# Kernel optimization log

Hardware: AMD Instinct MI355X
Metric: run time of the kernel (lower is better)

Reference implementation:

```python
import jax, jax.numpy as jnp
import numpy as np
from jax import lax

B, T, HID = 2, 2048, 2048
H, DK, DV = 16, 64, 128          # num_heads, head_k_dim, head_v_dim
C = 16                            # chunk_size (hardcoded in module __call__)
LOWR = 16                         # gate_low_rank_dim
NORMALIZER = 16.0                 # gate_logit_normalizer
EPS = 1e-5
SCALE = DK ** -0.5


def setup_inputs() -> dict:
    key = jax.random.key(0)
    ks = jax.random.split(key, 9)
    def w(k, shape):
        return jax.random.normal(k, shape, jnp.float32) * (shape[0] ** -0.5)
    return {
        "hidden_states": jax.random.normal(ks[0], (B, T, HID), jnp.float32),
        "Wq": w(ks[1], (HID, H * DK)),
        "Wk": w(ks[2], (HID, H * DK)),
        "Wv": w(ks[3], (HID, H * DV)),
        "Wg": w(ks[4], (HID, H * DV)),
        "Wgk1": w(ks[5], (HID, LOWR)),
        "Wgk2": w(ks[6], (LOWR, H * DK)),
        "bgk2": jnp.zeros((H * DK,), jnp.float32),
        "Wo": w(ks[7], (H * DV, HID)),
        "norm_w": jnp.ones((DV,), jnp.float32),
    }


def _chunk_gla(q, k, v, gk):
    """Chunked gated linear attention.
    q,k,gk: [B,T,H,DK], v: [B,T,H,DV]; gk is log-decay (<= 0).
    Recurrence: S_t = diag(exp(gk_t)) S_{t-1} + k_t^T v_t ; o_t = scale * q_t S_t.
    """
    b, t, h, dk = q.shape
    dv = v.shape[-1]
    n = t // C
    def to_chunks(x):  # [B,T,H,d] -> [B,H,N,C,d]
        return x.reshape(b, n, C, h, x.shape[-1]).transpose(0, 3, 1, 2, 4)
    q, k, v, gk = map(to_chunks, (q, k, v, gk))

    gc = jnp.cumsum(gk, axis=3)                 # within-chunk cumulative log-decay
    qe = q * jnp.exp(gc) * SCALE                # decay-weighted queries
    ke = k * jnp.exp(-gc)                       # inverse-decay keys (safe for C=16)
    # intra-chunk causal attention: A[i,j] = sum_d q_i k_j exp(gc_i - gc_j), j<=i
    A = jnp.einsum('bhncd,bhnmd->bhncm', qe, ke)
    A = jnp.where(jnp.tril(jnp.ones((C, C), bool)), A, 0.0)
    o_intra = jnp.einsum('bhncm,bhnme->bhnce', A, v)

    g_last = gc[:, :, :, -1:, :]                # [B,H,N,1,DK]
    k_dec = k * jnp.exp(g_last - gc)            # keys decayed to end of chunk
    kv = jnp.einsum('bhncd,bhnce->bhnde', k_dec, v)   # per-chunk state increment
    decay = jnp.exp(g_last[:, :, :, 0, :])      # [B,H,N,DK] total chunk decay

    def step(S, inp):  # S: [B,H,DK,DV]
        qe_c, kv_c, dec_c = inp
        o_c = jnp.einsum('bhcd,bhde->bhce', qe_c, S)
        return dec_c[..., None] * S + kv_c, o_c

    S0 = jnp.zeros((b, h, dk, dv), q.dtype)
    xs = (qe.transpose(2, 0, 1, 3, 4), kv.transpose(2, 0, 1, 3, 4), decay.transpose(2, 0, 1, 3))
    _, o_inter = lax.scan(step, S0, xs)          # [N,B,H,C,DV]

    o = o_intra + o_inter.transpose(1, 2, 0, 3, 4)
    return o.transpose(0, 2, 3, 1, 4).reshape(b, t, h, dv)  # [B,T,H,DV]


def reference(hidden_states, Wq, Wk, Wv, Wg, Wgk1, Wgk2, bgk2, Wo, norm_w):
    x = hidden_states
    q = (x @ Wq).reshape(B, T, H, DK)
    k = (x @ Wk).reshape(B, T, H, DK)
    v = (x @ Wv).reshape(B, T, H, DV)
    gk = jax.nn.log_sigmoid((x @ Wgk1) @ Wgk2 + bgk2) / NORMALIZER
    gk = gk.reshape(B, T, H, DK)

    o = _chunk_gla(q, k, v, gk)                  # [B,T,H,DV]

    # FusedRMSNormGated: rmsnorm(o) * weight, gated by swish(g) per head
    g = (x @ Wg).reshape(B, T, H, DV)
    o = o * lax.rsqrt(jnp.mean(o * o, axis=-1, keepdims=True) + EPS) * norm_w
    o = o * (g * jax.nn.sigmoid(g))
    return o.reshape(B, T, H * DV) @ Wo
```

## Files before the change

kernel.cpp:

```cpp
#include <hip/hip_runtime.h>
#include <hip/hip_bf16.h>
#include <math.h>

#define B_    2
#define T_    2048
#define HID_  2048
#define H_    16
#define DK_   64
#define DV_   128
#define CC    16
#define NCHUNK (T_/CC)
#define NSEG  16
#define M_    (B_*T_)
#define SCALE_ 0.125f

typedef __attribute__((ext_vector_type(8))) __bf16 bf16x8;
typedef __attribute__((ext_vector_type(8))) unsigned short u16x8;
typedef __attribute__((ext_vector_type(4))) float f32x4;

__device__ __forceinline__ unsigned short f2bf(float f) {
  unsigned int u = __float_as_uint(f);
  u += 0x7fff + ((u >> 16) & 1);
  return (unsigned short)(u >> 16);
}
__device__ __forceinline__ float bf2f(unsigned short u) {
  return __uint_as_float(((unsigned int)u) << 16);
}

typedef const __attribute__((address_space(1))) void* as1cv;
typedef __attribute__((address_space(3))) void* as3v;
__device__ __forceinline__ void gload16(const void* g, void* l) {
  __builtin_amdgcn_global_load_lds((as1cv)g, (as3v)l, 16, 0, 0);
}

__global__ __launch_bounds__(256) void prep_kernel(const float* __restrict__ x,
                                                   unsigned short* __restrict__ xb,
                                                   const float* __restrict__ Wq,
                                                   const float* __restrict__ Wk,
                                                   const float* __restrict__ Wv,
                                                   const float* __restrict__ Wg,
                                                   const float* __restrict__ Wo,
                                                   unsigned short* __restrict__ WqkT,
                                                   unsigned short* __restrict__ WvgT,
                                                   unsigned short* __restrict__ WoT) {
  const int t = threadIdx.x;
  int id = blockIdx.x;
  if (id < 2048) {
    const float4* x4 = reinterpret_cast<const float4*>(x);
    ushort4* o4 = reinterpret_cast<ushort4*>(xb);
    const int base = id * 1024 + t;
    float4 f0 = x4[base];
    float4 f1 = x4[base + 256];
    float4 f2 = x4[base + 512];
    float4 f3 = x4[base + 768];
    ushort4 u0 = {f2bf(f0.x), f2bf(f0.y), f2bf(f0.z), f2bf(f0.w)};
    ushort4 u1 = {f2bf(f1.x), f2bf(f1.y), f2bf(f1.z), f2bf(f1.w)};
    ushort4 u2 = {f2bf(f2.x), f2bf(f2.y), f2bf(f2.z), f2bf(f2.w)};
    ushort4 u3 = {f2bf(f3.x), f2bf(f3.y), f2bf(f3.z), f2bf(f3.w)};
    o4[base] = u0; o4[base + 256] = u1; o4[base + 512] = u2; o4[base + 768] = u3;
    return;
  }
  id -= 2048;
  const float* in; unsigned short* out; int N;
  if (id < 512)        { in = Wq; out = WqkT;                         N = 1024; }
  else if (id < 1024)  { in = Wk; out = WqkT + (size_t)1024*2048;     N = 1024; id -= 512; }
  else if (id < 2048)  { in = Wv; out = WvgT;                         N = 2048; id -= 1024; }
  else if (id < 3072)  { in = Wg; out = WvgT + (size_t)2048*2048;     N = 2048; id -= 2048; }
  else                 { in = Wo; out = WoT;                          N = 2048; id -= 3072; }
  const int nx = N / 64;
  const int n0 = (id % nx) * 64;
  const int k0 = (id / nx) * 64;
  __shared__ float tl[64][65];
  const int kr = t >> 4;
  const int nq = t & 15;
  #pragma unroll
  for (int it = 0; it < 4; ++it) {
    int kk = it*16 + kr;
    float4 v = *reinterpret_cast<const float4*>(&in[(size_t)(k0 + kk) * N + n0 + nq*4]);
    tl[kk][nq*4+0] = v.x; tl[kk][nq*4+1] = v.y;
    tl[kk][nq*4+2] = v.z; tl[kk][nq*4+3] = v.w;
  }
  __syncthreads();
  const int nr = t >> 3;
  const int kq = t & 7;
  #pragma unroll
  for (int it = 0; it < 2; ++it) {
    int nn = it*32 + nr;
    u16x8 u;
    #pragma unroll
    for (int r = 0; r < 8; ++r) u[r] = f2bf(tl[kq*8 + r][nn]);
    *reinterpret_cast<u16x8*>(&out[(size_t)(n0 + nn) * 2048 + k0 + kq*8]) = u;
  }
}

__global__ __launch_bounds__(256) void lr_kernel(const float* __restrict__ x,
                                                 const float* __restrict__ w1,
                                                 const float* __restrict__ w2,
                                                 const float* __restrict__ bias,
                                                 float* __restrict__ gkout) {
  const int row0 = blockIdx.x * 4;
  const int t = threadIdx.x;
  __shared__ float part[4][4][17];
  __shared__ float t1s[4][16];
  const int r    = t >> 6;
  const int lane = t & 63;
  const int j    = lane & 15;
  const int p    = lane >> 4;
  const float* xr = x + (size_t)(row0 + r) * HID_;
  float acc = 0.f;
  const int k0 = p * 512;
  for (int kk = k0; kk < k0 + 512; kk += 4) {
    float4 xv = *reinterpret_cast<const float4*>(&xr[kk]);
    acc = fmaf(xv.x, w1[(kk+0)*16 + j], acc);
    acc = fmaf(xv.y, w1[(kk+1)*16 + j], acc);
    acc = fmaf(xv.z, w1[(kk+2)*16 + j], acc);
    acc = fmaf(xv.w, w1[(kk+3)*16 + j], acc);
  }
  part[r][p][j] = acc;
  __syncthreads();
  if (t < 64) {
    int rr = t >> 4, jj = t & 15;
    t1s[rr][jj] = part[rr][0][jj] + part[rr][1][jj] + part[rr][2][jj] + part[rr][3][jj];
  }
  __syncthreads();
  #pragma unroll
  for (int i = 0; i < 4; ++i) {
    int n = t + i * 256;
    float b0 = bias[n];
    float a0 = b0, a1 = b0, a2 = b0, a3 = b0;
    #pragma unroll
    for (int jj = 0; jj < 16; ++jj) {
      float wv = w2[jj * 1024 + n];
      a0 = fmaf(t1s[0][jj], wv, a0);
      a1 = fmaf(t1s[1][jj], wv, a1);
      a2 = fmaf(t1s[2][jj], wv, a2);
      a3 = fmaf(t1s[3][jj], wv, a3);
    }
    gkout[(size_t)(row0+0)*1024 + n] = (fminf(a0,0.f) - log1pf(expf(-fabsf(a0)))) * (1.f/16.f);
    gkout[(size_t)(row0+1)*1024 + n] = (fminf(a1,0.f) - log1pf(expf(-fabsf(a1)))) * (1.f/16.f);
    gkout[(size_t)(row0+2)*1024 + n] = (fminf(a2,0.f) - log1pf(expf(-fabsf(a2)))) * (1.f/16.f);
    gkout[(size_t)(row0+3)*1024 + n] = (fminf(a3,0.f) - log1pf(expf(-fabsf(a3)))) * (1.f/16.f);
  }
}

template<bool OBF>
__global__ __launch_bounds__(512, 2) void gemm256(const unsigned short* __restrict__ A,
                                                  const unsigned short* __restrict__ Bt,
                                                  void* __restrict__ Cv,
                                                  int M, int N, int K) {
  __shared__ char ldsb[131072];
  const int t    = threadIdx.x;
  const int lane = t & 63;
  const int wid  = t >> 6;
  const int wr   = wid >> 2;
  const int wc   = wid & 3;
  const int lr   = lane & 15;
  const int lk   = lane >> 4;
  int flat = blockIdx.y * gridDim.x + blockIdx.x;
  if (gridDim.x * gridDim.y == 256) flat = (flat & 7) * 32 + (flat >> 3);
  const int row0 = (flat / gridDim.x) * 256;
  const int col0 = (flat % gridDim.x) * 256;
  const int NKT  = K >> 6;
  const size_t K2 = (size_t)K * 2;

  const int r_s  = t >> 2;
  const int kx_s = ((t & 3) * 16) ^ (((t >> 5) & 1) << 5);

  const int ha = wr;
  const int hb = wc >> 1;
  const int rbl = (wc & 1) * 64;

  f32x4 acc[8][4];
  #pragma unroll
  for (int m = 0; m < 8; ++m)
    #pragma unroll
    for (int n = 0; n < 4; ++n) acc[m][n] = (f32x4){0.f, 0.f, 0.f, 0.f};

  auto stage_half = [&](int p, int o, int h, int kt) {
    const char* src = o ? (const char*)Bt : (const char*)A;
    const int R0 = (o ? col0 : row0) + h * 128;
    const char* g = src + (size_t)(R0 + r_s) * K2 + (size_t)kt * 128 + kx_s;
    char* l = ldsb + ((((p << 1) | o) << 1 | h) << 14) + t * 16;
    gload16(g, l);
    gload16(g + 64, l + 8192);
  };
  auto lda = [&](int p, int mf, int ks) -> bf16x8 {
    int r = mf * 16 + lr;
    int a = ((((p << 1) | 0) << 1 | ha) << 14) + ks * 8192 + r * 64 + lk * 16;
    a ^= ((r >> 3) & 1) << 5;
    return *(const bf16x8*)(ldsb + a);
  };
  auto ldb = [&](int p, int nf, int ks) -> bf16x8 {
    int r = rbl + nf * 16 + lr;
    int a = ((((p << 1) | 1) << 1 | hb) << 14) + ks * 8192 + r * 64 + lk * 16;
    a ^= ((r >> 3) & 1) << 5;
    return *(const bf16x8*)(ldsb + a);
  };

  stage_half(0, 1, 0, 0); stage_half(0, 1, 1, 0);
  stage_half(0, 0, 0, 0); stage_half(0, 0, 1, 0);
  if (1 < NKT) {
    stage_half(1, 1, 0, 1); stage_half(1, 1, 1, 1);
    stage_half(1, 0, 0, 1); stage_half(1, 0, 1, 1);
  }
  __builtin_amdgcn_sched_barrier(0);
  asm volatile("s_waitcnt vmcnt(8)" ::: "memory");
  __builtin_amdgcn_sched_barrier(0);
  __builtin_amdgcn_s_barrier();

  bf16x8 fa[4][2], fb[2][2], fb2[2][2];

  for (int kt = 0; kt < NKT; ++kt) {
    const int p = kt & 1;
    const bool st = (kt + 2 < NKT);
    #pragma unroll
    for (int m = 0; m < 4; ++m) { fa[m][0] = lda(p, m, 0); fa[m][1] = lda(p, m, 1); }
    __builtin_amdgcn_sched_barrier(0);
    #pragma unroll
    for (int n = 0; n < 2; ++n) { fb[n][0] = ldb(p, n, 0); fb[n][1] = ldb(p, n, 1); }
    __builtin_amdgcn_sched_barrier(0);
    #pragma unroll
    for (int n = 0; n < 2; ++n) { fb2[n][0] = ldb(p, n + 2, 0); fb2[n][1] = ldb(p, n + 2, 1); }
    __builtin_amdgcn_sched_barrier(0);
    asm volatile("s_waitcnt lgkmcnt(4)" ::: "memory");
    __builtin_amdgcn_sched_barrier(0);
    __builtin_amdgcn_s_setprio(1);
    #pragma unroll
    for (int m = 0; m < 4; ++m)
      #pragma unroll
      for (int n = 0; n < 2; ++n) {
        acc[m][n] = __builtin_amdgcn_mfma_f32_16x16x32_bf16(fa[m][0], fb[n][0], acc[m][n], 0, 0, 0);
        acc[m][n] = __builtin_amdgcn_mfma_f32_16x16x32_bf16(fa[m][1], fb[n][1], acc[m][n], 0, 0, 0);
      }
    __builtin_amdgcn_s_setprio(0);
    __builtin_amdgcn_sched_barrier(0);
    asm volatile("s_waitcnt lgkmcnt(0)" ::: "memory");
    __builtin_amdgcn_sched_barrier(0);
    __builtin_amdgcn_s_setprio(1);
    #pragma unroll
    for (int m = 0; m < 4; ++m)
      #pragma unroll
      for (int n = 0; n < 2; ++n) {
        acc[m][n+2] = __builtin_amdgcn_mfma_f32_16x16x32_bf16(fa[m][0], fb2[n][0], acc[m][n+2], 0, 0, 0);
        acc[m][n+2] = __builtin_amdgcn_mfma_f32_16x16x32_bf16(fa[m][1], fb2[n][1], acc[m][n+2], 0, 0, 0);
      }
    __builtin_amdgcn_s_setprio(0);
    __builtin_amdgcn_sched_barrier(0);
    __builtin_amdgcn_s_barrier();
    if (st) { stage_half(p, 1, 0, kt + 2); stage_half(p, 1, 1, kt + 2); }
    __builtin_amdgcn_sched_barrier(0);
    #pragma unroll
    for (int m = 0; m < 4; ++m) { fa[m][0] = lda(p, m + 4, 0); fa[m][1] = lda(p, m + 4, 1); }
    __builtin_amdgcn_sched_barrier(0);
    asm volatile("s_waitcnt lgkmcnt(0)" ::: "memory");
    __builtin_amdgcn_sched_barrier(0);
    __builtin_amdgcn_s_setprio(1);
    #pragma unroll
    for (int m = 0; m < 4; ++m)
      #pragma unroll
      for (int n = 0; n < 2; ++n) {
        acc[m+4][n] = __builtin_amdgcn_mfma_f32_16x16x32_bf16(fa[m][0], fb[n][0], acc[m+4][n], 0, 0, 0);
        acc[m+4][n] = __builtin_amdgcn_mfma_f32_16x16x32_bf16(fa[m][1], fb[n][1], acc[m+4][n], 0, 0, 0);
      }
    #pragma unroll
    for (int m = 0; m < 4; ++m)
      #pragma unroll
      for (int n = 0; n < 2; ++n) {
        acc[m+4][n+2] = __builtin_amdgcn_mfma_f32_16x16x32_bf16(fa[m][0], fb2[n][0], acc[m+4][n+2], 0, 0, 0);
        acc[m+4][n+2] = __builtin_amdgcn_mfma_f32_16x16x32_bf16(fa[m][1], fb2[n][1], acc[m+4][n+2], 0, 0, 0);
      }
    __builtin_amdgcn_s_setprio(0);
    __builtin_amdgcn_sched_barrier(0);
    __builtin_amdgcn_s_barrier();
    if (st) { stage_half(p, 0, 0, kt + 2); stage_half(p, 0, 1, kt + 2); }
    __builtin_amdgcn_sched_barrier(0);
    if (kt == NKT - 2) asm volatile("s_waitcnt vmcnt(0)" ::: "memory");
    else               asm volatile("s_waitcnt vmcnt(8)" ::: "memory");
    __builtin_amdgcn_sched_barrier(0);
    __builtin_amdgcn_s_barrier();
  }

  #pragma unroll
  for (int m = 0; m < 8; ++m) {
    int row = row0 + wr*128 + m*16 + lk*4;
    #pragma unroll
    for (int n = 0; n < 4; ++n) {
      int col = col0 + wc*64 + n*16 + lr;
      #pragma unroll
      for (int j = 0; j < 4; ++j) {
        if (OBF) ((unsigned short*)Cv)[(size_t)(row + j) * N + col] = f2bf(acc[m][n][j]);
        else     ((float*)Cv)[(size_t)(row + j) * N + col] = acc[m][n][j];
      }
    }
  }
}

template<bool OBF>
__global__ __launch_bounds__(512, 2) void gemm256x128(const unsigned short* __restrict__ A,
                                                      const unsigned short* __restrict__ Bt,
                                                      void* __restrict__ Cv,
                                                      int M, int N, int K) {
  __shared__ char ldsb[98304];
  const int t    = threadIdx.x;
  const int lane = t & 63;
  const int wid  = t >> 6;
  const int wr   = wid >> 1;
  const int wc   = wid & 1;
  const int lr   = lane & 15;
  const int lk   = lane >> 4;
  int flat = blockIdx.y * gridDim.x + blockIdx.x;
  if (gridDim.x * gridDim.y == 256) flat = (flat & 7) * 32 + (flat >> 3);
  const int row0 = (flat / gridDim.x) * 256;
  const int col0 = (flat % gridDim.x) * 128;
  const int NKT  = K >> 6;
  const size_t K2 = (size_t)K * 2;

  const int r_s  = t >> 2;
  const int kx_s = ((t & 3) * 16) ^ (((t >> 5) & 1) << 5);

  const int ha  = wr >> 1;
  const int ral = (wr & 1) * 64;
  const int rbl = wc * 64;

  f32x4 acc[4][4];
  #pragma unroll
  for (int m = 0; m < 4; ++m)
    #pragma unroll
    for (int n = 0; n < 4; ++n) acc[m][n] = (f32x4){0.f, 0.f, 0.f, 0.f};

  auto stage_slot = [&](int p, int slot, int kt) {
    const char* src = (slot == 2) ? (const char*)Bt : (const char*)A;
    const int R0 = (slot == 2) ? col0 : (row0 + slot * 128);
    const char* g = src + (size_t)(R0 + r_s) * K2 + (size_t)kt * 128 + kx_s;
    char* l = ldsb + p * 49152 + slot * 16384 + t * 16;
    gload16(g, l);
    gload16(g + 64, l + 8192);
  };
  auto lda = [&](int p, int mf, int ks) -> bf16x8 {
    int r = ral + mf * 16 + lr;
    int a = p * 49152 + ha * 16384 + ks * 8192 + r * 64 + lk * 16;
    a ^= ((r >> 3) & 1) << 5;
    return *(const bf16x8*)(ldsb + a);
  };
  auto ldb = [&](int p, int nf, int ks) -> bf16x8 {
    int r = rbl + nf * 16 + lr;
    int a = p * 49152 + 32768 + ks * 8192 + r * 64 + lk * 16;
    a ^= ((r >> 3) & 1) << 5;
    return *(const bf16x8*)(ldsb + a);
  };

  stage_slot(0, 2, 0); stage_slot(0, 0, 0); stage_slot(0, 1, 0);
  if (1 < NKT) { stage_slot(1, 2, 1); stage_slot(1, 0, 1); stage_slot(1, 1, 1); }
  __builtin_amdgcn_sched_barrier(0);
  asm volatile("s_waitcnt vmcnt(6)" ::: "memory");
  __builtin_amdgcn_sched_barrier(0);
  __builtin_amdgcn_s_barrier();

  bf16x8 fa[2][2], fb[2][2], fb2[2][2];

  for (int kt = 0; kt < NKT; ++kt) {
    const int p = kt & 1;
    const bool st = (kt + 2 < NKT);
    #pragma unroll
    for (int m = 0; m < 2; ++m) { fa[m][0] = lda(p, m, 0); fa[m][1] = lda(p, m, 1); }
    __builtin_amdgcn_sched_barrier(0);
    #pragma unroll
    for (int n = 0; n < 2; ++n) { fb[n][0] = ldb(p, n, 0); fb[n][1] = ldb(p, n, 1); }
    __builtin_amdgcn_sched_barrier(0);
    #pragma unroll
    for (int n = 0; n < 2; ++n) { fb2[n][0] = ldb(p, n + 2, 0); fb2[n][1] = ldb(p, n + 2, 1); }
    __builtin_amdgcn_sched_barrier(0);
    asm volatile("s_waitcnt lgkmcnt(4)" ::: "memory");
    __builtin_amdgcn_sched_barrier(0);
    __builtin_amdgcn_s_setprio(1);
    #pragma unroll
    for (int m = 0; m < 2; ++m)
      #pragma unroll
      for (int n = 0; n < 2; ++n) {
        acc[m][n] = __builtin_amdgcn_mfma_f32_16x16x32_bf16(fa[m][0], fb[n][0], acc[m][n], 0, 0, 0);
        acc[m][n] = __builtin_amdgcn_mfma_f32_16x16x32_bf16(fa[m][1], fb[n][1], acc[m][n], 0, 0, 0);
      }
    __builtin_amdgcn_s_setprio(0);
    __builtin_amdgcn_sched_barrier(0);
    asm volatile("s_waitcnt lgkmcnt(0)" ::: "memory");
    __builtin_amdgcn_sched_barrier(0);
    __builtin_amdgcn_s_setprio(1);
    #pragma unroll
    for (int m = 0; m < 2; ++m)
      #pragma unroll
      for (int n = 0; n < 2; ++n) {
        acc[m][n+2] = __builtin_amdgcn_mfma_f32_16x16x32_bf16(fa[m][0], fb2[n][0], acc[m][n+2], 0, 0, 0);
        acc[m][n+2] = __builtin_amdgcn_mfma_f32_16x16x32_bf16(fa[m][1], fb2[n][1], acc[m][n+2], 0, 0, 0);
      }
    __builtin_amdgcn_s_setprio(0);
    __builtin_amdgcn_sched_barrier(0);
    __builtin_amdgcn_s_barrier();
    if (st) stage_slot(p, 2, kt + 2);
    __builtin_amdgcn_sched_barrier(0);
    #pragma unroll
    for (int m = 0; m < 2; ++m) { fa[m][0] = lda(p, m + 2, 0); fa[m][1] = lda(p, m + 2, 1); }
    __builtin_amdgcn_sched_barrier(0);
    asm volatile("s_waitcnt lgkmcnt(0)" ::: "memory");
    __builtin_amdgcn_sched_barrier(0);
    __builtin_amdgcn_s_setprio(1);
    #pragma unroll
    for (int m = 0; m < 2; ++m)
      #pragma unroll
      for (int n = 0; n < 2; ++n) {
        acc[m+2][n] = __builtin_amdgcn_mfma_f32_16x16x32_bf16(fa[m][0], fb[n][0], acc[m+2][n], 0, 0, 0);
        acc[m+2][n] = __builtin_amdgcn_mfma_f32_16x16x32_bf16(fa[m][1], fb[n][1], acc[m+2][n], 0, 0, 0);
      }
    #pragma unroll
    for (int m = 0; m < 2; ++m)
      #pragma unroll
      for (int n = 0; n < 2; ++n) {
        acc[m+2][n+2] = __builtin_amdgcn_mfma_f32_16x16x32_bf16(fa[m][0], fb2[n][0], acc[m+2][n+2], 0, 0, 0);
        acc[m+2][n+2] = __builtin_amdgcn_mfma_f32_16x16x32_bf16(fa[m][1], fb2[n][1], acc[m+2][n+2], 0, 0, 0);
      }
    __builtin_amdgcn_s_setprio(0);
    __builtin_amdgcn_sched_barrier(0);
    __builtin_amdgcn_s_barrier();
    if (st) { stage_slot(p, 0, kt + 2); stage_slot(p, 1, kt + 2); }
    __builtin_amdgcn_sched_barrier(0);
    if (kt == NKT - 2) asm volatile("s_waitcnt vmcnt(0)" ::: "memory");
    else               asm volatile("s_waitcnt vmcnt(6)" ::: "memory");
    __builtin_amdgcn_sched_barrier(0);
    __builtin_amdgcn_s_barrier();
  }

  #pragma unroll
  for (int m = 0; m < 4; ++m) {
    int row = row0 + wr*64 + m*16 + lk*4;
    #pragma unroll
    for (int n = 0; n < 4; ++n) {
      int col = col0 + wc*64 + n*16 + lr;
      #pragma unroll
      for (int j = 0; j < 4; ++j) {
        if (OBF) ((unsigned short*)Cv)[(size_t)(row + j) * N + col] = f2bf(acc[m][n][j]);
        else     ((float*)Cv)[(size_t)(row + j) * N + col] = acc[m][n][j];
      }
    }
  }
}

__global__ __launch_bounds__(256) void gla_phase_a(const float* __restrict__ qk,
                                                   const unsigned short* __restrict__ vg,
                                                   const float* __restrict__ gk,
                                                   float* __restrict__ Sseg,
                                                   float* __restrict__ Dseg) {
  const int seg = blockIdx.x & 15;
  const int h   = (blockIdx.x >> 4) & 15;
  const int b   = blockIdx.x >> 8;
  const int t    = threadIdx.x;
  const int lane = t & 63;
  const int wid  = t >> 6;
  const int q    = lane >> 4;
  const int lr   = lane & 15;
  __shared__ float gc[16][68];
  __shared__ float dec_[64];
  __shared__ unsigned short kdT[64][40];
  __shared__ unsigned short vvT[128][40];

  for (int i = t; i < 1024; i += 256) kdT[i >> 4][16 + (i & 15)] = 0;
  for (int i = t; i < 2048; i += 256) vvT[i >> 4][16 + (i & 15)] = 0;

  f32x4 s_reg[2][4];
  #pragma unroll
  for (int et = 0; et < 2; ++et)
    #pragma unroll
    for (int dt = 0; dt < 4; ++dt) s_reg[et][dt] = (f32x4){0.f,0.f,0.f,0.f};
  float gt = 0.f;

  for (int c8 = 0; c8 < NCHUNK/NSEG; ++c8) {
    const int ch = seg * (NCHUNK/NSEG) + c8;
    __syncthreads();
    {
      float acc = 0.f;
      #pragma unroll
      for (int c = 0; c < CC; ++c) {
        acc += gk[((size_t)(b*T_ + ch*CC + c)) * 1024 + h*DK_ + lane];
        gc[c][lane] = acc;
      }
      gt += acc;
      dec_[lane] = expf(acc);
    }
    __syncthreads();
    {
      int c = t >> 4, d0 = (t & 15) * 4;
      float4 k4 = *reinterpret_cast<const float4*>(
          &qk[((size_t)(b*T_ + ch*CC + c)) * 2048 + 1024 + h*DK_ + d0]);
      float ka[4] = {k4.x, k4.y, k4.z, k4.w};
      #pragma unroll
      for (int j = 0; j < 4; ++j)
        kdT[d0 + j][c] = f2bf(ka[j] * expf(gc[CC-1][d0 + j] - gc[c][d0 + j]));
    }
    {
      int c = t & 15, e0 = (t >> 4) * 8;
      const ushort4* vp = reinterpret_cast<const ushort4*>(
          &vg[((size_t)(b*T_ + ch*CC + c)) * 4096 + h*DV_ + e0]);
      ushort4 a = vp[0], bb = vp[1];
      vvT[e0+0][c] = a.x;  vvT[e0+1][c] = a.y;  vvT[e0+2][c] = a.z;  vvT[e0+3][c] = a.w;
      vvT[e0+4][c] = bb.x; vvT[e0+5][c] = bb.y; vvT[e0+6][c] = bb.z; vvT[e0+7][c] = bb.w;
    }
    __syncthreads();
    bf16x8 vf[2], kf[4];
    #pragma unroll
    for (int et = 0; et < 2; ++et)
      vf[et] = *(const bf16x8*)&vvT[wid*32 + et*16 + lr][q*8];
    #pragma unroll
    for (int dt = 0; dt < 4; ++dt)
      kf[dt] = *(const bf16x8*)&kdT[dt*16 + lr][q*8];
    #pragma unroll
    for (int et = 0; et < 2; ++et)
      #pragma unroll
      for (int dt = 0; dt < 4; ++dt) {
        f32x4 dl = __builtin_amdgcn_mfma_f32_16x16x32_bf16(vf[et], kf[dt],
                     (f32x4){0.f,0.f,0.f,0.f}, 0, 0, 0);
        float dv = dec_[dt*16 + lr];
        #pragma unroll
        for (int j = 0; j < 4; ++j)
          s_reg[et][dt][j] = fmaf(s_reg[et][dt][j], dv, dl[j]);
      }
  }
  const size_t base = ((size_t)((b*H_ + h)*NSEG + seg)) * (DK_*DV_);
  #pragma unroll
  for (int et = 0; et < 2; ++et)
    #pragma unroll
    for (int dt = 0; dt < 4; ++dt)
      #pragma unroll
      for (int j = 0; j < 4; ++j)
        Sseg[base + (size_t)(wid*32 + et*16 + q*4 + j) * 64 + dt*16 + lr] = s_reg[et][dt][j];
  if (t < 64)
    Dseg[(size_t)((b*H_ + h)*NSEG + seg) * DK_ + t] = expf(gt);
}

__global__ __launch_bounds__(256) void gla_combine(float* __restrict__ Sseg,
                                                   const float* __restrict__ Dseg) {
  const int bh = blockIdx.x;
  const int t = threadIdx.x;
  __shared__ float Dl[64];
  float4 S_run[8];
  #pragma unroll
  for (int j = 0; j < 8; ++j) S_run[j] = (float4){0.f,0.f,0.f,0.f};
  const int d0 = (t * 4) & 63;
  for (int seg = 0; seg < NSEG; ++seg) {
    const size_t base = ((size_t)bh*NSEG + seg) * (DK_*DV_);
    if (t < 64) Dl[t] = Dseg[((size_t)bh*NSEG + seg) * DK_ + t];
    __syncthreads();
    #pragma unroll
    for (int j = 0; j < 8; ++j) {
      int idx = j*1024 + t*4;
      float4 sl = *reinterpret_cast<float4*>(&Sseg[base + idx]);
      *reinterpret_cast<float4*>(&Sseg[base + idx]) = S_run[j];
      S_run[j].x = fmaf(Dl[d0+0], S_run[j].x, sl.x);
      S_run[j].y = fmaf(Dl[d0+1], S_run[j].y, sl.y);
      S_run[j].z = fmaf(Dl[d0+2], S_run[j].z, sl.z);
      S_run[j].w = fmaf(Dl[d0+3], S_run[j].w, sl.w);
    }
    __syncthreads();
  }
}

__global__ __launch_bounds__(256) void gla_phase_c(const float* __restrict__ qk,
                                                   const unsigned short* __restrict__ vg,
                                                   const float* __restrict__ gk,
                                                   const float* __restrict__ Sseg,
                                                   const float* __restrict__ norm_w,
                                                   unsigned short* __restrict__ yb) {
  const int seg = blockIdx.x & 15;
  const int h   = (blockIdx.x >> 4) & 15;
  const int b   = blockIdx.x >> 8;
  const int t    = threadIdx.x;
  const int lane = t & 63;
  const int wid  = t >> 6;
  const int q    = lane >> 4;
  const int lr   = lane & 15;
  __shared__ float gc[16][68];
  __shared__ float dec_[64];
  __shared__ unsigned short qe[16][72];
  __shared__ unsigned short ke[16][72];
  __shared__ unsigned short kdT[64][40];
  __shared__ unsigned short vvT[128][40];
  __shared__ unsigned short Am[16][40];
  __shared__ unsigned short Sb[128][72];
  __shared__ float ss_lds[4][16];
  __shared__ float nw[128];

  for (int i = t; i < 1024; i += 256) kdT[i >> 4][16 + (i & 15)] = 0;
  for (int i = t; i < 2048; i += 256) vvT[i >> 4][16 + (i & 15)] = 0;
  if (t < 256) { int c = t >> 4, m = t & 15; Am[c][16 + m] = 0; }
  if (t < 128) nw[t] = norm_w[t];

  f32x4 s_reg[2][4];
  const size_t sbase = ((size_t)((b*H_ + h)*NSEG + seg)) * (DK_*DV_);
  #pragma unroll
  for (int et = 0; et < 2; ++et)
    #pragma unroll
    for (int dt = 0; dt < 4; ++dt)
      #pragma unroll
      for (int j = 0; j < 4; ++j) {
        int e = wid*32 + et*16 + q*4 + j, d = dt*16 + lr;
        float v = Sseg[sbase + (size_t)e * 64 + d];
        s_reg[et][dt][j] = v;
        Sb[e][d] = f2bf(v);
      }

  for (int c8 = 0; c8 < NCHUNK/NSEG; ++c8) {
    const int ch = seg * (NCHUNK/NSEG) + c8;
    __syncthreads();
    {
      float acc = 0.f;
      #pragma unroll
      for (int c = 0; c < CC; ++c) {
        acc += gk[((size_t)(b*T_ + ch*CC + c)) * 1024 + h*DK_ + lane];
        gc[c][lane] = acc;
      }
      dec_[lane] = expf(acc);
    }
    __syncthreads();
    {
      int c = t >> 4, d0 = (t & 15) * 4;
      const size_t gbq = ((size_t)(b*T_ + ch*CC + c)) * 2048 + h*DK_ + d0;
      float4 q4 = *reinterpret_cast<const float4*>(&qk[gbq]);
      float4 k4 = *reinterpret_cast<const float4*>(&qk[gbq + 1024]);
      float qa[4] = {q4.x, q4.y, q4.z, q4.w};
      float ka[4] = {k4.x, k4.y, k4.z, k4.w};
      ushort4 qw, kw;
      unsigned short* qwp = (unsigned short*)&qw;
      unsigned short* kwp = (unsigned short*)&kw;
      #pragma unroll
      for (int j = 0; j < 4; ++j) {
        float gcv = gc[c][d0 + j];
        float gl  = gc[CC-1][d0 + j];
        qwp[j] = f2bf(qa[j] * expf(gcv) * SCALE_);
        kwp[j] = f2bf(ka[j] * expf(-gcv));
        kdT[d0 + j][c] = f2bf(ka[j] * expf(gl - gcv));
      }
      *reinterpret_cast<ushort4*>(&qe[c][d0]) = qw;
      *reinterpret_cast<ushort4*>(&ke[c][d0]) = kw;
    }
    {
      int c = t & 15, e0 = (t >> 4) * 8;
      const ushort4* vp = reinterpret_cast<const ushort4*>(
          &vg[((size_t)(b*T_ + ch*CC + c)) * 4096 + h*DV_ + e0]);
      ushort4 a = vp[0], bb = vp[1];
      vvT[e0+0][c] = a.x;  vvT[e0+1][c] = a.y;  vvT[e0+2][c] = a.z;  vvT[e0+3][c] = a.w;
      vvT[e0+4][c] = bb.x; vvT[e0+5][c] = bb.y; vvT[e0+6][c] = bb.z; vvT[e0+7][c] = bb.w;
    }
    __syncthreads();
    bf16x8 qA0 = *(const bf16x8*)&qe[lr][q*8];
    bf16x8 qA1 = *(const bf16x8*)&qe[lr][32 + q*8];
    {
      bf16x8 kB0 = *(const bf16x8*)&ke[lr][q*8];
      bf16x8 kB1 = *(const bf16x8*)&ke[lr][32 + q*8];
      f32x4 accA = __builtin_amdgcn_mfma_f32_16x16x32_bf16(qA0, kB0,
                     (f32x4){0.f,0.f,0.f,0.f}, 0, 0, 0);
      accA = __builtin_amdgcn_mfma_f32_16x16x32_bf16(qA1, kB1, accA, 0, 0, 0);
      #pragma unroll
      for (int j = 0; j < 4; ++j) {
        int c = q*4 + j;
        Am[c][lr] = (lr <= c) ? f2bf(accA[j]) : (unsigned short)0;
      }
    }
    bf16x8 vf[2], kf[4];
    #pragma unroll
    for (int et = 0; et < 2; ++et)
      vf[et] = *(const bf16x8*)&vvT[wid*32 + et*16 + lr][q*8];
    #pragma unroll
    for (int dt = 0; dt < 4; ++dt)
      kf[dt] = *(const bf16x8*)&kdT[dt*16 + lr][q*8];
    #pragma unroll
    for (int et = 0; et < 2; ++et)
      #pragma unroll
      for (int dt = 0; dt < 4; ++dt) {
        f32x4 dl = __builtin_amdgcn_mfma_f32_16x16x32_bf16(vf[et], kf[dt],
                     (f32x4){0.f,0.f,0.f,0.f}, 0, 0, 0);
        float dv = dec_[dt*16 + lr];
        #pragma unroll
        for (int j = 0; j < 4; ++j)
          s_reg[et][dt][j] = fmaf(s_reg[et][dt][j], dv, dl[j]);
      }
    __syncthreads();
    {
      bf16x8 amA = *(const bf16x8*)&Am[lr][q*8];
      f32x4 accO[2];
      #pragma unroll
      for (int et = 0; et < 2; ++et) {
        int e0 = wid*32 + et*16;
        bf16x8 sB0 = *(const bf16x8*)&Sb[e0 + lr][q*8];
        bf16x8 sB1 = *(const bf16x8*)&Sb[e0 + lr][32 + q*8];
        accO[et] = __builtin_amdgcn_mfma_f32_16x16x32_bf16(qA0, sB0,
                     (f32x4){0.f,0.f,0.f,0.f}, 0, 0, 0);
        accO[et] = __builtin_amdgcn_mfma_f32_16x16x32_bf16(qA1, sB1, accO[et], 0, 0, 0);
        accO[et] = __builtin_amdgcn_mfma_f32_16x16x32_bf16(amA, vf[et], accO[et], 0, 0, 0);
      }
      #pragma unroll
      for (int j = 0; j < 4; ++j) {
        float pj = accO[0][j]*accO[0][j] + accO[1][j]*accO[1][j];
        pj += __shfl_xor(pj, 1, 64);
        pj += __shfl_xor(pj, 2, 64);
        pj += __shfl_xor(pj, 4, 64);
        pj += __shfl_xor(pj, 8, 64);
        if (lr == 0) ss_lds[wid][q*4 + j] = pj;
      }
      __syncthreads();
      #pragma unroll
      for (int j = 0; j < 4; ++j) {
        int r = q*4 + j;
        float tot = ss_lds[0][r] + ss_lds[1][r] + ss_lds[2][r] + ss_lds[3][r];
        float inv = rsqrtf(tot * (1.f/128.f) + 1e-5f);
        const size_t rowg = (size_t)(b*T_ + ch*CC + r);
        #pragma unroll
        for (int et = 0; et < 2; ++et) {
          int e = wid*32 + et*16 + lr;
          float gv = bf2f(vg[rowg * 4096 + 2048 + h*DV_ + e]);
          float si = gv / (1.f + expf(-gv));
          yb[rowg * 2048 + h*DV_ + e] = f2bf(accO[et][j] * inv * nw[e] * si);
        }
      }
    }
    __syncthreads();
    #pragma unroll
    for (int et = 0; et < 2; ++et)
      #pragma unroll
      for (int dt = 0; dt < 4; ++dt)
        #pragma unroll
        for (int j = 0; j < 4; ++j)
          Sb[wid*32 + et*16 + q*4 + j][dt*16 + lr] = f2bf(s_reg[et][dt][j]);
  }
}

extern "C" void kernel_launch(void* const* d_in, const int* in_sizes, int n_in,
                              void* d_out, int out_size, void* d_ws, size_t ws_size,
                              hipStream_t stream) {
  const float* x      = (const float*)d_in[0];
  const float* Wq     = (const float*)d_in[1];
  const float* Wk     = (const float*)d_in[2];
  const float* Wv     = (const float*)d_in[3];
  const float* Wg     = (const float*)d_in[4];
  const float* Wgk1   = (const float*)d_in[5];
  const float* Wgk2   = (const float*)d_in[6];
  const float* bgk2   = (const float*)d_in[7];
  const float* Wo     = (const float*)d_in[8];
  const float* norm_w = (const float*)d_in[9];
  float* out = (float*)d_out;
  float* ws  = (float*)d_ws;

  float*          qk   = ws;
  float*          gkb  = ws + 8388608;
  unsigned short* vg   = (unsigned short*)(ws + 12582912);
  float*          wbuf = ws + 20971520;
  float*          Sseg = ws + 29360128;
  float*          Dseg = ws + 33554432;
  unsigned short* WoT  = (unsigned short*)(ws + 33652736);

  unsigned short* WqkT = (unsigned short*)wbuf;
  unsigned short* WvgT = (unsigned short*)(wbuf + 2097152);
  unsigned short* xb   = (unsigned short*)(wbuf + 6291456);
  unsigned short* yb   = (unsigned short*)wbuf;

  dim3 blk(256);
  prep_kernel<<<dim3(6144), blk, 0, stream>>>(x, xb, Wq, Wk, Wv, Wg, Wo, WqkT, WvgT, WoT);
  lr_kernel<<<dim3(1024), blk, 0, stream>>>(x, Wgk1, Wgk2, bgk2, gkb);
  gemm256x128<false><<<dim3(2048/128, 4096/256), dim3(512), 0, stream>>>(xb, WqkT, qk, M_, 2048, HID_);
  gemm256<true     ><<<dim3(4096/256, 4096/256), dim3(512), 0, stream>>>(xb, WvgT, vg, M_, 4096, HID_);
  gla_phase_a<<<B_*H_*NSEG, blk, 0, stream>>>(qk, vg, gkb, Sseg, Dseg);
  gla_combine<<<B_*H_, blk, 0, stream>>>(Sseg, Dseg);
  gla_phase_c<<<B_*H_*NSEG, blk, 0, stream>>>(qk, vg, gkb, Sseg, norm_w, yb);
  gemm256x128<false><<<dim3(2048/128, 4096/256), dim3(512), 0, stream>>>(yb, WoT, out, M_, HID_, HID_);
}
```

Measured before the change: 291.1 us.

## Store q/k projection in bf16 and loosen GEMM scheduling barriers

The q/k projection GEMM now writes bf16 output instead of fp32. Both GLA phase kernels read that bf16 buffer and widen it to float, which halves the memory traffic for that intermediate on both the write and the reads. The GEMM main loops also drop most manual sched_barrier and explicit lgkmcnt waits, leaving the compiler to interleave LDS loads with MFMAs. The risks are slightly lower precision for q and k before the decay weighting, and a compiler-chosen schedule that may overlap LDS loads and MFMAs worse than the hand-tuned one.

```diff
diff --git a/kernel.cpp b/kernel.cpp
--- a/kernel.cpp
+++ b/kernel.cpp
@@ -203,10 +203,9 @@
     stage_half(1, 1, 0, 1); stage_half(1, 1, 1, 1);
     stage_half(1, 0, 0, 1); stage_half(1, 0, 1, 1);
   }
+  asm volatile("s_waitcnt vmcnt(8)" ::: "memory");
+  __builtin_amdgcn_s_barrier();
   __builtin_amdgcn_sched_barrier(0);
-  asm volatile("s_waitcnt vmcnt(8)" ::: "memory");
-  __builtin_amdgcn_sched_barrier(0);
-  __builtin_amdgcn_s_barrier();
 
   bf16x8 fa[4][2], fb[2][2], fb2[2][2];
 
@@ -215,15 +214,10 @@
     const bool st = (kt + 2 < NKT);
     #pragma unroll
     for (int m = 0; m < 4; ++m) { fa[m][0] = lda(p, m, 0); fa[m][1] = lda(p, m, 1); }
-    __builtin_amdgcn_sched_barrier(0);
     #pragma unroll
     for (int n = 0; n < 2; ++n) { fb[n][0] = ldb(p, n, 0); fb[n][1] = ldb(p, n, 1); }
-    __builtin_amdgcn_sched_barrier(0);
     #pragma unroll
     for (int n = 0; n < 2; ++n) { fb2[n][0] = ldb(p, n + 2, 0); fb2[n][1] = ldb(p, n + 2, 1); }
-    __builtin_amdgcn_sched_barrier(0);
-    asm volatile("s_waitcnt lgkmcnt(4)" ::: "memory");
-    __builtin_amdgcn_sched_barrier(0);
     __builtin_amdgcn_s_setprio(1);
     #pragma unroll
     for (int m = 0; m < 4; ++m)
@@ -232,11 +226,6 @@
         acc[m][n] = __builtin_amdgcn_mfma_f32_16x16x32_bf16(fa[m][0], fb[n][0], acc[m][n], 0, 0, 0);
         acc[m][n] = __builtin_amdgcn_mfma_f32_16x16x32_bf16(fa[m][1], fb[n][1], acc[m][n], 0, 0, 0);
       }
-    __builtin_amdgcn_s_setprio(0);
-    __builtin_amdgcn_sched_barrier(0);
-    asm volatile("s_waitcnt lgkmcnt(0)" ::: "memory");
-    __builtin_amdgcn_sched_barrier(0);
-    __builtin_amdgcn_s_setprio(1);
     #pragma unroll
     for (int m = 0; m < 4; ++m)
       #pragma unroll
@@ -247,13 +236,10 @@
     __builtin_amdgcn_s_setprio(0);
     __builtin_amdgcn_sched_barrier(0);
     __builtin_amdgcn_s_barrier();
+    __builtin_amdgcn_sched_barrier(0);
     if (st) { stage_half(p, 1, 0, kt + 2); stage_half(p, 1, 1, kt + 2); }
-    __builtin_amdgcn_sched_barrier(0);
     #pragma unroll
     for (int m = 0; m < 4; ++m) { fa[m][0] = lda(p, m + 4, 0); fa[m][1] = lda(p, m + 4, 1); }
-    __builtin_amdgcn_sched_barrier(0);
-    asm volatile("s_waitcnt lgkmcnt(0)" ::: "memory");
-    __builtin_amdgcn_sched_barrier(0);
     __builtin_amdgcn_s_setprio(1);
     #pragma unroll
     for (int m = 0; m < 4; ++m)
@@ -272,12 +258,12 @@
     __builtin_amdgcn_s_setprio(0);
     __builtin_amdgcn_sched_barrier(0);
     __builtin_amdgcn_s_barrier();
+    __builtin_amdgcn_sched_barrier(0);
     if (st) { stage_half(p, 0, 0, kt + 2); stage_half(p, 0, 1, kt + 2); }
-    __builtin_amdgcn_sched_barrier(0);
     if (kt == NKT - 2) asm volatile("s_waitcnt vmcnt(0)" ::: "memory");
     else               asm volatile("s_waitcnt vmcnt(8)" ::: "memory");
-    __builtin_amdgcn_sched_barrier(0);
     __builtin_amdgcn_s_barrier();
+    __builtin_amdgcn_sched_barrier(0);
   }
 
   #pragma unroll
@@ -351,10 +337,9 @@
 
   stage_slot(0, 2, 0); stage_slot(0, 0, 0); stage_slot(0, 1, 0);
   if (1 < NKT) { stage_slot(1, 2, 1); stage_slot(1, 0, 1); stage_slot(1, 1, 1); }
+  asm volatile("s_waitcnt vmcnt(6)" ::: "memory");
+  __builtin_amdgcn_s_barrier();
   __builtin_amdgcn_sched_barrier(0);
-  asm volatile("s_waitcnt vmcnt(6)" ::: "memory");
-  __builtin_amdgcn_sched_barrier(0);
-  __builtin_amdgcn_s_barrier();
 
   bf16x8 fa[2][2], fb[2][2], fb2[2][2];
 
@@ -363,15 +348,10 @@
     const bool st = (kt + 2 < NKT);
     #pragma unroll
     for (int m = 0; m < 2; ++m) { fa[m][0] = lda(p, m, 0); fa[m][1] = lda(p, m, 1); }
-    __builtin_amdgcn_sched_barrier(0);
     #pragma unroll
     for (int n = 0; n < 2; ++n) { fb[n][0] = ldb(p, n, 0); fb[n][1] = ldb(p, n, 1); }
-    __builtin_amdgcn_sched_barrier(0);
     #pragma unroll
     for (int n = 0; n < 2; ++n) { fb2[n][0] = ldb(p, n + 2, 0); fb2[n][1] = ldb(p, n + 2, 1); }
-    __builtin_amdgcn_sched_barrier(0);
-    asm volatile("s_waitcnt lgkmcnt(4)" ::: "memory");
-    __builtin_amdgcn_sched_barrier(0);
     __builtin_amdgcn_s_setprio(1);
     #pragma unroll
     for (int m = 0; m < 2; ++m)
@@ -380,11 +360,6 @@
         acc[m][n] = __builtin_amdgcn_mfma_f32_16x16x32_bf16(fa[m][0], fb[n][0], acc[m][n], 0, 0, 0);
         acc[m][n] = __builtin_amdgcn_mfma_f32_16x16x32_bf16(fa[m][1], fb[n][1], acc[m][n], 0, 0, 0);
       }
-    __builtin_amdgcn_s_setprio(0);
-    __builtin_amdgcn_sched_barrier(0);
-    asm volatile("s_waitcnt lgkmcnt(0)" ::: "memory");
-    __builtin_amdgcn_sched_barrier(0);
-    __builtin_amdgcn_s_setprio(1);
     #pragma unroll
     for (int m = 0; m < 2; ++m)
       #pragma unroll
@@ -395,13 +370,10 @@
     __builtin_amdgcn_s_setprio(0);
     __builtin_amdgcn_sched_barrier(0);
     __builtin_amdgcn_s_barrier();
+    __builtin_amdgcn_sched_barrier(0);
     if (st) stage_slot(p, 2, kt + 2);
-    __builtin_amdgcn_sched_barrier(0);
     #pragma unroll
     for (int m = 0; m < 2; ++m) { fa[m][0] = lda(p, m + 2, 0); fa[m][1] = lda(p, m + 2, 1); }
-    __builtin_amdgcn_sched_barrier(0);
-    asm volatile("s_waitcnt lgkmcnt(0)" ::: "memory");
-    __builtin_amdgcn_sched_barrier(0);
     __builtin_amdgcn_s_setprio(1);
     #pragma unroll
     for (int m = 0; m < 2; ++m)
@@ -420,12 +392,12 @@
     __builtin_amdgcn_s_setprio(0);
     __builtin_amdgcn_sched_barrier(0);
     __builtin_amdgcn_s_barrier();
+    __builtin_amdgcn_sched_barrier(0);
     if (st) { stage_slot(p, 0, kt + 2); stage_slot(p, 1, kt + 2); }
-    __builtin_amdgcn_sched_barrier(0);
     if (kt == NKT - 2) asm volatile("s_waitcnt vmcnt(0)" ::: "memory");
     else               asm volatile("s_waitcnt vmcnt(6)" ::: "memory");
-    __builtin_amdgcn_sched_barrier(0);
     __builtin_amdgcn_s_barrier();
+    __builtin_amdgcn_sched_barrier(0);
   }
 
   #pragma unroll
@@ -443,7 +415,7 @@
   }
 }
 
-__global__ __launch_bounds__(256) void gla_phase_a(const float* __restrict__ qk,
+__global__ __launch_bounds__(256) void gla_phase_a(const unsigned short* __restrict__ qkb,
                                                    const unsigned short* __restrict__ vg,
                                                    const float* __restrict__ gk,
                                                    float* __restrict__ Sseg,
@@ -487,9 +459,9 @@
     __syncthreads();
     {
       int c = t >> 4, d0 = (t & 15) * 4;
-      float4 k4 = *reinterpret_cast<const float4*>(
-          &qk[((size_t)(b*T_ + ch*CC + c)) * 2048 + 1024 + h*DK_ + d0]);
-      float ka[4] = {k4.x, k4.y, k4.z, k4.w};
+      ushort4 k4u = *reinterpret_cast<const ushort4*>(
+          &qkb[((size_t)(b*T_ + ch*CC + c)) * 2048 + 1024 + h*DK_ + d0]);
+      float ka[4] = {bf2f(k4u.x), bf2f(k4u.y), bf2f(k4u.z), bf2f(k4u.w)};
       #pragma unroll
       for (int j = 0; j < 4; ++j)
         kdT[d0 + j][c] = f2bf(ka[j] * expf(gc[CC-1][d0 + j] - gc[c][d0 + j]));
@@ -561,7 +533,7 @@
   }
 }
 
-__global__ __launch_bounds__(256) void gla_phase_c(const float* __restrict__ qk,
+__global__ __launch_bounds__(256) void gla_phase_c(const unsigned short* __restrict__ qkb,
                                                    const unsigned short* __restrict__ vg,
                                                    const float* __restrict__ gk,
                                                    const float* __restrict__ Sseg,
@@ -621,10 +593,10 @@
     {
       int c = t >> 4, d0 = (t & 15) * 4;
       const size_t gbq = ((size_t)(b*T_ + ch*CC + c)) * 2048 + h*DK_ + d0;
-      float4 q4 = *reinterpret_cast<const float4*>(&qk[gbq]);
-      float4 k4 = *reinterpret_cast<const float4*>(&qk[gbq + 1024]);
-      float qa[4] = {q4.x, q4.y, q4.z, q4.w};
-      float ka[4] = {k4.x, k4.y, k4.z, k4.w};
+      ushort4 q4u = *reinterpret_cast<const ushort4*>(&qkb[gbq]);
+      ushort4 k4u = *reinterpret_cast<const ushort4*>(&qkb[gbq + 1024]);
+      float qa[4] = {bf2f(q4u.x), bf2f(q4u.y), bf2f(q4u.z), bf2f(q4u.w)};
+      float ka[4] = {bf2f(k4u.x), bf2f(k4u.y), bf2f(k4u.z), bf2f(k4u.w)};
       ushort4 qw, kw;
       unsigned short* qwp = (unsigned short*)&qw;
       unsigned short* kwp = (unsigned short*)&kw;
@@ -746,7 +718,7 @@
   float* out = (float*)d_out;
   float* ws  = (float*)d_ws;
 
-  float*          qk   = ws;
+  unsigned short* qkb  = (unsigned short*)ws;
   float*          gkb  = ws + 8388608;
   unsigned short* vg   = (unsigned short*)(ws + 12582912);
   float*          wbuf = ws + 20971520;
@@ -762,10 +734,10 @@
   dim3 blk(256);
   prep_kernel<<<dim3(6144), blk, 0, stream>>>(x, xb, Wq, Wk, Wv, Wg, Wo, WqkT, WvgT, WoT);
   lr_kernel<<<dim3(1024), blk, 0, stream>>>(x, Wgk1, Wgk2, bgk2, gkb);
-  gemm256x128<false><<<dim3(2048/128, 4096/256), dim3(512), 0, stream>>>(xb, WqkT, qk, M_, 2048, HID_);
+  gemm256x128<true ><<<dim3(2048/128, 4096/256), dim3(512), 0, stream>>>(xb, WqkT, qkb, M_, 2048, HID_);
   gemm256<true     ><<<dim3(4096/256, 4096/256), dim3(512), 0, stream>>>(xb, WvgT, vg, M_, 4096, HID_);
-  gla_phase_a<<<B_*H_*NSEG, blk, 0, stream>>>(qk, vg, gkb, Sseg, Dseg);
+  gla_phase_a<<<B_*H_*NSEG, blk, 0, stream>>>(qkb, vg, gkb, Sseg, Dseg);
   gla_combine<<<B_*H_, blk, 0, stream>>>(Sseg, Dseg);
-  gla_phase_c<<<B_*H_*NSEG, blk, 0, stream>>>(qk, vg, gkb, Sseg, norm_w, yb);
+  gla_phase_c<<<B_*H_*NSEG, blk, 0, stream>>>(qkb, vg, gkb, Sseg, norm_w, yb);
   gemm256x128<false><<<dim3(2048/128, 4096/256), dim3(512), 0, stream>>>(yb, WoT, out, M_, HID_, HID_);
 }
```

Result: no change. 291.2 us (+0.1%).
